# Kernel tuning notes

Hardware: AMD Instinct MI355X
Metric: run time of the kernel (lower is better)

Reference implementation:

```python
import jax, jax.numpy as jnp
import numpy as np

NHEAD = 12
EPS = 1e-5


def layernorm_nobias(x, gamma):
    mu = jnp.mean(x, axis=-1, keepdims=True)
    var = jnp.var(x, axis=-1, keepdims=True)
    return (x - mu) * jax.lax.rsqrt(var + EPS) * gamma


def setup_inputs() -> dict:
    key = jax.random.key(0)
    ks = jax.random.split(key, 10)
    b, l, d = 4, 2048, 768
    s = d ** -0.5
    return {
        "x": jax.random.normal(ks[0], (b, l, d), jnp.float32),
        "Wq": jax.random.normal(ks[1], (d, d), jnp.float32) * s,
        "Wk": jax.random.normal(ks[2], (d, d), jnp.float32) * s,
        "bk": jax.random.normal(ks[3], (d,), jnp.float32) * 0.02,
        "Wv": jax.random.normal(ks[4], (d, d), jnp.float32) * s,
        "bv": jax.random.normal(ks[5], (d,), jnp.float32) * 0.02,
        "gq": jnp.ones((d,), jnp.float32),
        "gk": jnp.ones((d,), jnp.float32),
        "Wo": jax.random.normal(ks[6], (d, d), jnp.float32) * s,
        "bo": jnp.zeros((d,), jnp.float32),
    }


def reference(x, Wq, Wk, bk, Wv, bv, gq, gk, Wo, bo):
    b, l, d = x.shape
    n = NHEAD
    hd = d // n
    scale = hd ** -0.5
    # projections (torch Linear: x @ W.T + b), QK-norm over full dmodel
    q = layernorm_nobias(x @ Wq.T, gq)
    k = layernorm_nobias(x @ Wk.T + bk, gk)
    v = x @ Wv.T + bv
    # split heads: b l (n hd) -> b n l hd
    q = q.reshape(b, l, n, hd).transpose(0, 2, 1, 3)
    k = k.reshape(b, l, n, hd).transpose(0, 2, 1, 3)
    v = v.reshape(b, l, n, hd).transpose(0, 2, 1, 3)
    # scores [b, n, l_q, l_k]; NOTE: softmax over the QUERY axis (dim=-2)
    scores = jnp.einsum('bnqd,bnkd->bnqk', q, k) * scale
    attn = jax.nn.softmax(scores, axis=-2)
    o = jnp.einsum('bnqk,bnkd->bnqd', attn, v)
    o = o.transpose(0, 2, 1, 3).reshape(b, l, d)
    return o @ Wo.T + bo + x
```

## Files before the change

kernel.cpp:

```cpp
#include <hip/hip_runtime.h>
#include <cstddef>
#include <cstdint>


typedef unsigned short u16;
typedef short  bf16x8 __attribute__((ext_vector_type(8)));
typedef float  f32x4  __attribute__((ext_vector_type(4)));
typedef unsigned short u16x8 __attribute__((ext_vector_type(8)));
typedef unsigned short u16x4 __attribute__((ext_vector_type(4)));

#define B_   4
#define L_   2048
#define D_   768
#define NH_  12
#define HD_  64
#define M_   (B_*L_)
#define SC2  (0.125f * 1.44269504088896f)

__device__ __forceinline__ float ex2(float x) { return __builtin_amdgcn_exp2f(x); }

__device__ __forceinline__ u16 f2bf(float f) {
    union { float f; unsigned u; } v; v.f = f;
    unsigned r = v.u + 0x7FFFu + ((v.u >> 16) & 1u);
    return (u16)(r >> 16);
}
__device__ __forceinline__ float bf2f(u16 b) {
    union { unsigned u; float f; } v; v.u = ((unsigned)b) << 16;
    return v.f;
}
__device__ __forceinline__ unsigned fbits(float f) {
    union { float f; unsigned u; } v; v.f = f; return v.u;
}
__device__ __forceinline__ unsigned packbf(float lo, float hi) {
    return __builtin_amdgcn_perm(fbits(hi), fbits(lo), 0x07060302u);
}

__device__ __forceinline__ void gld16(const void* g, void* l) {
    __builtin_amdgcn_global_load_lds(
        (const __attribute__((address_space(1))) unsigned*)g,
        (__attribute__((address_space(3))) unsigned*)l, 16, 0, 0);
}

__global__ __launch_bounds__(256) void cvt_bf16_kernel(
    const float* __restrict__ X, u16* __restrict__ Y, int n8)
{
    int i = blockIdx.x * 256 + threadIdx.x;
    if (i >= n8) return;
    const float4* xp = (const float4*)X + (size_t)i * 2;
    float4 a = xp[0], b = xp[1];
    u16x8 o;
    o[0] = f2bf(a.x); o[1] = f2bf(a.y); o[2] = f2bf(a.z); o[3] = f2bf(a.w);
    o[4] = f2bf(b.x); o[5] = f2bf(b.y); o[6] = f2bf(b.z); o[7] = f2bf(b.w);
    *((u16x8*)Y + i) = o;
}

__global__ __launch_bounds__(256) void cvt4_bf16_kernel(
    const float* __restrict__ W0, const float* __restrict__ W1,
    const float* __restrict__ W2, const float* __restrict__ W3,
    u16* __restrict__ Y0, u16* __restrict__ Y1,
    u16* __restrict__ Y2, u16* __restrict__ Y3, int n8)
{
    const float* X; u16* Y;
    switch (blockIdx.y) {
        case 0: X = W0; Y = Y0; break;
        case 1: X = W1; Y = Y1; break;
        case 2: X = W2; Y = Y2; break;
        default: X = W3; Y = Y3; break;
    }
    int i = blockIdx.x * 256 + threadIdx.x;
    if (i >= n8) return;
    const float4* xp = (const float4*)X + (size_t)i * 2;
    float4 a = xp[0], b = xp[1];
    u16x8 o;
    o[0] = f2bf(a.x); o[1] = f2bf(a.y); o[2] = f2bf(a.z); o[3] = f2bf(a.w);
    o[4] = f2bf(b.x); o[5] = f2bf(b.y); o[6] = f2bf(b.z); o[7] = f2bf(b.w);
    *((u16x8*)Y + i) = o;
}

__global__ __launch_bounds__(256) void gemm_qkv(
    const u16* __restrict__ A,
    const u16* __restrict__ W0, const u16* __restrict__ W1,
    const u16* __restrict__ W2,
    const float* __restrict__ bk, const float* __restrict__ bv,
    float* __restrict__ q32, float* __restrict__ k32, u16* __restrict__ vb)
{
    __shared__ __align__(16) u16 As[128 * 32];
    __shared__ __align__(16) u16 Bs[128 * 32];
    const int tid  = threadIdx.x;
    const int lane = tid & 63, w = tid >> 6;
    const int s    = lane & 15, quad = lane >> 4;
    const int seg  = blockIdx.x / 6;
    const int bn   = (blockIdx.x % 6) * 128;
    const int bm   = blockIdx.y * 128;
    const u16* W = (seg == 0) ? W0 : ((seg == 1) ? W1 : W2);
    const int mh = (w >> 1) * 64, nh = (w & 1) * 64;
    const int wb = tid & ~63;
    f32x4 acc[4][4];
    #pragma unroll
    for (int i = 0; i < 4; ++i)
        #pragma unroll
        for (int j = 0; j < 4; ++j) acc[i][j] = (f32x4){0.f, 0.f, 0.f, 0.f};

    for (int k0 = 0; k0 < D_; k0 += 32) {
        {
            int c = tid, r = c >> 2, cc = c & 3;
            gld16(A + (size_t)(bm + r) * D_ + k0 + cc * 8, As + (size_t)wb * 8);
            gld16(W + (size_t)(bn + r) * D_ + k0 + cc * 8, Bs + (size_t)wb * 8);
            c = tid + 256; r = c >> 2; cc = c & 3;
            gld16(A + (size_t)(bm + r) * D_ + k0 + cc * 8, As + (size_t)(wb + 256) * 8);
            gld16(W + (size_t)(bn + r) * D_ + k0 + cc * 8, Bs + (size_t)(wb + 256) * 8);
        }
        __syncthreads();
        bf16x8 af[4], bf[4];
        #pragma unroll
        for (int i = 0; i < 4; ++i)
            af[i] = *(const bf16x8*)(As + (mh + i * 16 + s) * 32 + quad * 8);
        #pragma unroll
        for (int j = 0; j < 4; ++j)
            bf[j] = *(const bf16x8*)(Bs + (nh + j * 16 + s) * 32 + quad * 8);
        #pragma unroll
        for (int i = 0; i < 4; ++i)
            #pragma unroll
            for (int j = 0; j < 4; ++j)
                acc[i][j] = __builtin_amdgcn_mfma_f32_16x16x32_bf16(
                    af[i], bf[j], acc[i][j], 0, 0, 0);
        __syncthreads();
    }
    #pragma unroll
    for (int j = 0; j < 4; ++j) {
        const int n = bn + nh + j * 16 + s;
        float bb = 0.0f;
        if (seg == 1) bb = bk[n];
        else if (seg == 2) bb = bv[n];
        #pragma unroll
        for (int i = 0; i < 4; ++i) {
            const int m0 = bm + mh + i * 16 + quad * 4;
            #pragma unroll
            for (int r = 0; r < 4; ++r) {
                float y = acc[i][j][r] + bb;
                const size_t idx = (size_t)(m0 + r) * D_ + n;
                if (seg == 0)      q32[idx] = y;
                else if (seg == 1) k32[idx] = y;
                else               vb[idx]  = f2bf(y);
            }
        }
    }
}

__global__ __launch_bounds__(256) void gemm_final(
    const u16* __restrict__ A, const u16* __restrict__ W,
    const float* __restrict__ bias, const float* __restrict__ resid,
    float* __restrict__ outf)
{
    __shared__ __align__(16) u16 As[128 * 32];
    __shared__ __align__(16) u16 Bs[128 * 32];
    const int tid  = threadIdx.x;
    const int lane = tid & 63, w = tid >> 6;
    const int s    = lane & 15, quad = lane >> 4;
    const int bm   = blockIdx.y * 128, bn = blockIdx.x * 128;
    const int mh   = (w >> 1) * 64, nh = (w & 1) * 64;
    const int wb   = tid & ~63;
    f32x4 acc[4][4];
    #pragma unroll
    for (int i = 0; i < 4; ++i)
        #pragma unroll
        for (int j = 0; j < 4; ++j) acc[i][j] = (f32x4){0.f, 0.f, 0.f, 0.f};

    for (int k0 = 0; k0 < D_; k0 += 32) {
        {
            int c = tid, r = c >> 2, cc = c & 3;
            gld16(A + (size_t)(bm + r) * D_ + k0 + cc * 8, As + (size_t)wb * 8);
            gld16(W + (size_t)(bn + r) * D_ + k0 + cc * 8, Bs + (size_t)wb * 8);
            c = tid + 256; r = c >> 2; cc = c & 3;
            gld16(A + (size_t)(bm + r) * D_ + k0 + cc * 8, As + (size_t)(wb + 256) * 8);
            gld16(W + (size_t)(bn + r) * D_ + k0 + cc * 8, Bs + (size_t)(wb + 256) * 8);
        }
        __syncthreads();
        bf16x8 af[4], bf[4];
        #pragma unroll
        for (int i = 0; i < 4; ++i)
            af[i] = *(const bf16x8*)(As + (mh + i * 16 + s) * 32 + quad * 8);
        #pragma unroll
        for (int j = 0; j < 4; ++j)
            bf[j] = *(const bf16x8*)(Bs + (nh + j * 16 + s) * 32 + quad * 8);
        #pragma unroll
        for (int i = 0; i < 4; ++i)
            #pragma unroll
            for (int j = 0; j < 4; ++j)
                acc[i][j] = __builtin_amdgcn_mfma_f32_16x16x32_bf16(
                    af[i], bf[j], acc[i][j], 0, 0, 0);
        __syncthreads();
    }
    #pragma unroll
    for (int j = 0; j < 4; ++j) {
        const int n = bn + nh + j * 16 + s;
        const float bb = bias[n];
        #pragma unroll
        for (int i = 0; i < 4; ++i) {
            const int m0 = bm + mh + i * 16 + quad * 4;
            #pragma unroll
            for (int r = 0; r < 4; ++r) {
                const size_t idx = (size_t)(m0 + r) * D_ + n;
                outf[idx] = acc[i][j][r] + bb + resid[idx];
            }
        }
    }
}

__global__ __launch_bounds__(256) void ln_bf16(
    const float* __restrict__ X, const float* __restrict__ gamma,
    u16* __restrict__ Y, float scale)
{
    const int row = blockIdx.x;
    const float* x = X + (size_t)row * D_;
    const int tid = threadIdx.x;
    float v[3];
    float lsum = 0.f, lsq = 0.f;
    #pragma unroll
    for (int e = 0; e < 3; ++e) {
        float t = x[tid + e * 256];
        v[e] = t; lsum += t; lsq += t * t;
    }
    #pragma unroll
    for (int off = 32; off > 0; off >>= 1) {
        lsum += __shfl_down(lsum, off);
        lsq  += __shfl_down(lsq,  off);
    }
    __shared__ float s1[4], s2[4];
    const int wv = tid >> 6, lane = tid & 63;
    if (lane == 0) { s1[wv] = lsum; s2[wv] = lsq; }
    __syncthreads();
    const float sum = s1[0] + s1[1] + s1[2] + s1[3];
    const float sq  = s2[0] + s2[1] + s2[2] + s2[3];
    const float mu  = sum * (1.0f / D_);
    const float var = sq * (1.0f / D_) - mu * mu;
    const float inv = rsqrtf(var + 1e-5f) * scale;
    #pragma unroll
    for (int e = 0; e < 3; ++e) {
        int c = tid + e * 256;
        Y[(size_t)row * D_ + c] = f2bf((v[e] - mu) * inv * gamma[c]);
    }
}

__global__ __launch_bounds__(256) void attn_stats(
    const u16* __restrict__ Qb, const u16* __restrict__ Kb,
    float* __restrict__ Rl)
{
    __shared__ __align__(16) u16 Ks[128 * 64];
    __shared__ __align__(16) u16 Qs[2][128 * 64];
    __shared__ float lbuf[4][64];
    const int tid  = threadIdx.x;
    const int lane = tid & 63, w = tid >> 6;
    const int s    = lane & 15, quad = lane >> 4;
    const int s7   = s & 7;
    const int bh   = blockIdx.y;
    const int b    = bh / NH_, h = bh % NH_;
    const int kbase = blockIdx.x * 128;
    const u16* Qg = Qb + (size_t)b * L_ * D_ + h * HD_;
    const u16* Kg = Kb + (size_t)b * L_ * D_ + h * HD_;
    const int mh = (w >> 1) * 64;
    const int nh = (w & 1) * 64;
    const int wb = tid & ~63;

    #pragma unroll
    for (int c0 = 0; c0 < 1024; c0 += 256) {
        int c = c0 + tid, r = c >> 3, cc = (c & 7) ^ (r & 7);
        gld16(Kg + (size_t)(kbase + r) * D_ + cc * 8, Ks + (size_t)(c0 + wb) * 8);
        gld16(Qg + (size_t)r * D_ + cc * 8, Qs[0] + (size_t)(c0 + wb) * 8);
    }
    __syncthreads();
    bf16x8 kf[2][4];
    #pragma unroll
    for (int kk = 0; kk < 2; ++kk)
        #pragma unroll
        for (int i = 0; i < 4; ++i)
            kf[kk][i] = *(const bf16x8*)(Ks + (mh + i * 16 + s) * 64 +
                                         ((kk * 4 + quad) ^ s7) * 8);
    float lacc[4][4];
    #pragma unroll
    for (int i = 0; i < 4; ++i)
        #pragma unroll
        for (int r = 0; r < 4; ++r) lacc[i][r] = 0.f;

    for (int t = 0; t < 16; ++t) {
        if (t < 15) {
            const int qn = (t + 1) * 128;
            u16* Qd = Qs[(t + 1) & 1];
            #pragma unroll
            for (int c0 = 0; c0 < 1024; c0 += 256) {
                int c = c0 + tid, r = c >> 3, cc = (c & 7) ^ (r & 7);
                gld16(Qg + (size_t)(qn + r) * D_ + cc * 8, Qd + (size_t)(c0 + wb) * 8);
            }
        }
        const u16* Qt = Qs[t & 1];
        f32x4 acc[4][4];
        #pragma unroll
        for (int i = 0; i < 4; ++i)
            #pragma unroll
            for (int j = 0; j < 4; ++j) acc[i][j] = (f32x4){0.f, 0.f, 0.f, 0.f};
        #pragma unroll
        for (int kk = 0; kk < 2; ++kk) {
            bf16x8 bf[4];
            #pragma unroll
            for (int j = 0; j < 4; ++j)
                bf[j] = *(const bf16x8*)(Qt + (nh + j * 16 + s) * 64 +
                                         ((kk * 4 + quad) ^ s7) * 8);
            #pragma unroll
            for (int i = 0; i < 4; ++i)
                #pragma unroll
                for (int j = 0; j < 4; ++j)
                    acc[i][j] = __builtin_amdgcn_mfma_f32_16x16x32_bf16(
                        kf[kk][i], bf[j], acc[i][j], 0, 0, 0);
        }
        #pragma unroll
        for (int i = 0; i < 4; ++i)
            #pragma unroll
            for (int r = 0; r < 4; ++r) {
                float l0 = ex2(acc[i][0][r]) + ex2(acc[i][1][r]);
                float l1 = ex2(acc[i][2][r]) + ex2(acc[i][3][r]);
                lacc[i][r] += l0 + l1;
            }
        __syncthreads();
    }
    #pragma unroll
    for (int i = 0; i < 4; ++i)
        #pragma unroll
        for (int r = 0; r < 4; ++r) {
            float v = lacc[i][r];
            #pragma unroll
            for (int d2 = 1; d2 < 16; d2 <<= 1) v += __shfl_xor(v, d2);
            lacc[i][r] = v;
        }
    if (s == 0) {
        #pragma unroll
        for (int i = 0; i < 4; ++i)
            #pragma unroll
            for (int r = 0; r < 4; ++r)
                lbuf[w][i * 16 + quad * 4 + r] = lacc[i][r];
    }
    __syncthreads();
    if (tid < 128) {
        int kh = tid >> 6, kl = tid & 63;
        float l = lbuf[kh * 2][kl] + lbuf[kh * 2 + 1][kl];
        Rl[(size_t)bh * L_ + kbase + tid] = 1.0f / l;
    }
}

__global__ __launch_bounds__(256) void transpose_v_scaled(
    const u16* __restrict__ Vb, const float* __restrict__ Rl,
    u16* __restrict__ Vt)
{
    const int l0 = blockIdx.x * 64, h = blockIdx.y, b = blockIdx.z;
    const int bh = b * NH_ + h;
    __shared__ __align__(16) u16 Ts[64][72];
    const int tid = threadIdx.x;
    #pragma unroll
    for (int c = tid; c < 512; c += 256) {
        int r = c >> 3, cc = c & 7;
        u16x8 val = *(const u16x8*)(Vb + (size_t)(b * L_ + l0 + r) * D_ + h * HD_ + cc * 8);
        const float rl = Rl[(size_t)bh * L_ + l0 + r];
        #pragma unroll
        for (int e = 0; e < 8; ++e) val[e] = f2bf(bf2f(val[e]) * rl);
        *(u16x8*)(&Ts[r][cc * 8]) = val;
    }
    __syncthreads();
    const int d = tid >> 2, lc = (tid & 3) * 16;
    u16 tmp[16];
    #pragma unroll
    for (int e = 0; e < 16; ++e) tmp[e] = Ts[lc + e][d];
    u16* dst = Vt + ((size_t)bh * HD_ + d) * L_ + l0 + (lc & 32) + ((lc >> 4) & 1) * 4;
    #pragma unroll
    for (int qd = 0; qd < 4; ++qd) {
        u16x4 o;
        #pragma unroll
        for (int e = 0; e < 4; ++e) o[e] = tmp[qd * 4 + e];
        *(u16x4*)(dst + qd * 8) = o;
    }
}

__global__ __launch_bounds__(256, 2) void attn_out(
    const u16* __restrict__ Qb, const u16* __restrict__ Kb,
    const u16* __restrict__ Vt, u16* __restrict__ Ob)
{
    __shared__ __align__(16) u16 Qs[256 * 64];
    __shared__ __align__(16) u16 Ks[2][64 * 64];
    __shared__ __align__(16) u16 Vts[2][64 * 64];
    const int tid  = threadIdx.x;
    const int lane = tid & 63, w = tid >> 6;
    const int s    = lane & 15, quad = lane >> 4;
    const int s7   = s & 7;
    const int bh   = blockIdx.y;
    const int b    = bh / NH_, h = bh % NH_;
    const int qbase = blockIdx.x * 256;
    const int qw   = w * 64;
    const u16* Qg = Qb + (size_t)b * L_ * D_ + h * HD_;
    const u16* Kg = Kb + (size_t)b * L_ * D_ + h * HD_;
    const u16* Vg = Vt + (size_t)bh * HD_ * L_;
    const int wb = tid & ~63;

    #pragma unroll
    for (int c0 = 0; c0 < 2048; c0 += 256) {
        int c = c0 + tid, r = c >> 3, cc = (c & 7) ^ (r & 7);
        gld16(Qg + (size_t)(qbase + r) * D_ + cc * 8, Qs + (size_t)(c0 + wb) * 8);
    }
    {
        int c = tid, r = c >> 3, cc = (c & 7) ^ (r & 7);
        gld16(Kg + (size_t)r * D_ + cc * 8, Ks[0] + (size_t)wb * 8);
        gld16(Vg + (size_t)r * L_ + cc * 8, Vts[0] + (size_t)wb * 8);
        c = tid + 256; r = c >> 3; cc = (c & 7) ^ (r & 7);
        gld16(Kg + (size_t)r * D_ + cc * 8, Ks[0] + (size_t)(wb + 256) * 8);
        gld16(Vg + (size_t)r * L_ + cc * 8, Vts[0] + (size_t)(wb + 256) * 8);
    }
    __syncthreads();
    bf16x8 qf[2][4];
    #pragma unroll
    for (int kk = 0; kk < 2; ++kk)
        #pragma unroll
        for (int j = 0; j < 4; ++j)
            qf[kk][j] = *(const bf16x8*)(Qs + (qw + j * 16 + s) * 64 +
                                         ((kk * 4 + quad) ^ s7) * 8);
    f32x4 acc_o[4][4];
    #pragma unroll
    for (int i = 0; i < 4; ++i)
        #pragma unroll
        for (int j = 0; j < 4; ++j) acc_o[i][j] = (f32x4){0.f, 0.f, 0.f, 0.f};

    for (int t = 0; t < 32; ++t) {
        const u16* Kt  = Ks[t & 1];
        const u16* Vtt = Vts[t & 1];
        if (t < 31) {
            const int kn = (t + 1) * 64;
            u16* Kd = Ks[(t + 1) & 1];
            u16* Vd = Vts[(t + 1) & 1];
            int c = tid, r = c >> 3, cc = (c & 7) ^ (r & 7);
            gld16(Kg + (size_t)(kn + r) * D_ + cc * 8, Kd + (size_t)wb * 8);
            gld16(Vg + (size_t)r * L_ + kn + cc * 8,   Vd + (size_t)wb * 8);
            c = tid + 256; r = c >> 3; cc = (c & 7) ^ (r & 7);
            gld16(Kg + (size_t)(kn + r) * D_ + cc * 8, Kd + (size_t)(wb + 256) * 8);
            gld16(Vg + (size_t)r * L_ + kn + cc * 8,   Vd + (size_t)(wb + 256) * 8);
        }
        f32x4 acc_s[4][4];
        #pragma unroll
        for (int i = 0; i < 4; ++i)
            #pragma unroll
            for (int j = 0; j < 4; ++j) acc_s[i][j] = (f32x4){0.f, 0.f, 0.f, 0.f};
        #pragma unroll
        for (int kk = 0; kk < 2; ++kk) {
            bf16x8 kfr[4];
            #pragma unroll
            for (int i = 0; i < 4; ++i)
                kfr[i] = *(const bf16x8*)(Kt + (i * 16 + s) * 64 +
                                          ((kk * 4 + quad) ^ s7) * 8);
            #pragma unroll
            for (int i = 0; i < 4; ++i)
                #pragma unroll
                for (int j = 0; j < 4; ++j)
                    acc_s[i][j] = __builtin_amdgcn_mfma_f32_16x16x32_bf16(
                        kfr[i], qf[kk][j], acc_s[i][j], 0, 0, 0);
        }
        unsigned pk[4][4][2];
        #pragma unroll
        for (int i = 0; i < 4; ++i)
            #pragma unroll
            for (int j = 0; j < 4; ++j) {
                float p0 = ex2(acc_s[i][j][0]), p1 = ex2(acc_s[i][j][1]);
                float p2 = ex2(acc_s[i][j][2]), p3 = ex2(acc_s[i][j][3]);
                pk[i][j][0] = packbf(p0, p1);
                pk[i][j][1] = packbf(p2, p3);
            }
        #pragma unroll
        for (int kk = 0; kk < 2; ++kk) {
            bf16x8 av[4];
            #pragma unroll
            for (int i = 0; i < 4; ++i)
                av[i] = *(const bf16x8*)(Vtt + (i * 16 + s) * 64 +
                                         ((kk * 4 + quad) ^ s7) * 8);
            #pragma unroll
            for (int j = 0; j < 4; ++j) {
                union { unsigned u[4]; bf16x8 v; } bu;
                bu.u[0] = pk[2 * kk][j][0];
                bu.u[1] = pk[2 * kk][j][1];
                bu.u[2] = pk[2 * kk + 1][j][0];
                bu.u[3] = pk[2 * kk + 1][j][1];
                #pragma unroll
                for (int i = 0; i < 4; ++i)
                    acc_o[i][j] = __builtin_amdgcn_mfma_f32_16x16x32_bf16(
                        av[i], bu.v, acc_o[i][j], 0, 0, 0);
            }
        }
        __syncthreads();
    }
    #pragma unroll
    for (int i = 0; i < 4; ++i) {
        const int d0 = i * 16 + quad * 4;
        const int dchunk = i * 2 + (quad >> 1), doff = (quad & 1) * 4;
        #pragma unroll
        for (int j = 0; j < 4; ++j) {
            const int q = qw + j * 16 + s;
            u16x4 ov;
            #pragma unroll
            for (int r = 0; r < 4; ++r) ov[r] = f2bf(acc_o[i][j][r]);
            *(u16x4*)(Qs + q * 64 + (dchunk ^ s7) * 8 + doff) = ov;
        }
    }
    __syncthreads();
    {
        const int q7 = tid & 7;
        u16* dst = Ob + (size_t)(b * L_ + qbase + tid) * D_ + h * HD_;
        #pragma unroll
        for (int c = 0; c < 8; ++c) {
            u16x8 v = *(const u16x8*)(Qs + tid * 64 + ((c ^ q7) * 8));
            *(u16x8*)(dst + c * 8) = v;
        }
    }
}

extern "C" void kernel_launch(void* const* d_in, const int* in_sizes, int n_in,
                              void* d_out, int out_size, void* d_ws, size_t ws_size,
                              hipStream_t stream)
{
    const float* x  = (const float*)d_in[0];
    const float* Wq = (const float*)d_in[1];
    const float* Wk = (const float*)d_in[2];
    const float* bk = (const float*)d_in[3];
    const float* Wv = (const float*)d_in[4];
    const float* bv = (const float*)d_in[5];
    const float* gq = (const float*)d_in[6];
    const float* gk = (const float*)d_in[7];
    const float* Wo = (const float*)d_in[8];
    const float* bo = (const float*)d_in[9];
    float* out = (float*)d_out;

    char* p = (char*)d_ws;
    float* q32 = (float*)p;  p += (size_t)M_ * D_ * 4;
    float* k32 = (float*)p;  p += (size_t)M_ * D_ * 4;
    u16* xb  = (u16*)p;      p += (size_t)M_ * D_ * 2;
    u16* qb  = (u16*)p;      p += (size_t)M_ * D_ * 2;
    u16* kb  = (u16*)p;      p += (size_t)M_ * D_ * 2;
    u16* vb  = (u16*)p;      p += (size_t)M_ * D_ * 2;
    u16* wqb = (u16*)p;      p += (size_t)D_ * D_ * 2;
    u16* wkb = (u16*)p;      p += (size_t)D_ * D_ * 2;
    u16* wvb = (u16*)p;      p += (size_t)D_ * D_ * 2;
    u16* wob = (u16*)p;      p += (size_t)D_ * D_ * 2;
    float* Rl = (float*)p;   p += (size_t)B_ * NH_ * L_ * 4;
    u16* ob = (u16*)q32;
    u16* vt = (u16*)k32;

    const int nX = M_ * D_, nW = D_ * D_;
    cvt_bf16_kernel<<<nX / 2048, 256, 0, stream>>>(x, xb, nX / 8);
    cvt4_bf16_kernel<<<dim3(nW / 2048, 4), 256, 0, stream>>>(
        Wq, Wk, Wv, Wo, wqb, wkb, wvb, wob, nW / 8);

    gemm_qkv<<<dim3(18, M_ / 128), 256, 0, stream>>>(
        xb, wqb, wkb, wvb, bk, bv, q32, k32, vb);

    ln_bf16<<<M_, 256, 0, stream>>>(q32, gq, qb, SC2);
    ln_bf16<<<M_, 256, 0, stream>>>(k32, gk, kb, 1.0f);

    dim3 sgrid(L_ / 128, B_ * NH_);
    attn_stats<<<sgrid, 256, 0, stream>>>(qb, kb, Rl);
    transpose_v_scaled<<<dim3(L_ / 64, NH_, B_), 256, 0, stream>>>(vb, Rl, vt);
    dim3 ogrid(L_ / 256, B_ * NH_);
    attn_out<<<ogrid, 256, 0, stream>>>(qb, kb, vt, ob);

    gemm_final<<<dim3(D_ / 128, M_ / 128), 256, 0, stream>>>(ob, wob, bo, x, out);
}
```

Measured before the change: 314.8 us.

## Double-buffer GEMM tiles, swizzle LDS, and store pre-norm Q/K in bf16

```diff
diff --git a/kernel.cpp b/kernel.cpp
--- a/kernel.cpp
+++ b/kernel.cpp
@@ -82,10 +82,10 @@
     const u16* __restrict__ W0, const u16* __restrict__ W1,
     const u16* __restrict__ W2,
     const float* __restrict__ bk, const float* __restrict__ bv,
-    float* __restrict__ q32, float* __restrict__ k32, u16* __restrict__ vb)
-{
-    __shared__ __align__(16) u16 As[128 * 32];
-    __shared__ __align__(16) u16 Bs[128 * 32];
+    u16* __restrict__ q_o, u16* __restrict__ k_o, u16* __restrict__ v_o)
+{
+    __shared__ __align__(16) u16 lds[16384];
+    __shared__ float bs[128];
     const int tid  = threadIdx.x;
     const int lane = tid & 63, w = tid >> 6;
     const int s    = lane & 15, quad = lane >> 4;
@@ -93,56 +93,83 @@
     const int bn   = (blockIdx.x % 6) * 128;
     const int bm   = blockIdx.y * 128;
     const u16* W = (seg == 0) ? W0 : ((seg == 1) ? W1 : W2);
+    u16* OUT = (seg == 0) ? q_o : ((seg == 1) ? k_o : v_o);
     const int mh = (w >> 1) * 64, nh = (w & 1) * 64;
     const int wb = tid & ~63;
+    const int cq = quad ^ ((s >> 1) & 3);
+
+    if (tid < 128)
+        bs[tid] = (seg == 1) ? bk[bn + tid] : ((seg == 2) ? bv[bn + tid] : 0.0f);
+
     f32x4 acc[4][4];
     #pragma unroll
-    for (int i = 0; i < 4; ++i)
-        #pragma unroll
-        for (int j = 0; j < 4; ++j) acc[i][j] = (f32x4){0.f, 0.f, 0.f, 0.f};
-
-    for (int k0 = 0; k0 < D_; k0 += 32) {
-        {
-            int c = tid, r = c >> 2, cc = c & 3;
-            gld16(A + (size_t)(bm + r) * D_ + k0 + cc * 8, As + (size_t)wb * 8);
-            gld16(W + (size_t)(bn + r) * D_ + k0 + cc * 8, Bs + (size_t)wb * 8);
-            c = tid + 256; r = c >> 2; cc = c & 3;
-            gld16(A + (size_t)(bm + r) * D_ + k0 + cc * 8, As + (size_t)(wb + 256) * 8);
-            gld16(W + (size_t)(bn + r) * D_ + k0 + cc * 8, Bs + (size_t)(wb + 256) * 8);
-        }
+    for (int j = 0; j < 4; ++j)
+        #pragma unroll
+        for (int i = 0; i < 4; ++i) acc[j][i] = (f32x4){0.f, 0.f, 0.f, 0.f};
+
+    {
+        int c = tid, r = c >> 2, cs = (c & 3) ^ ((r >> 1) & 3);
+        gld16(A + (size_t)(bm + r) * D_ + cs * 8, lds + (size_t)wb * 8);
+        gld16(W + (size_t)(bn + r) * D_ + cs * 8, lds + 8192 + (size_t)wb * 8);
+        c = tid + 256; r = c >> 2; cs = (c & 3) ^ ((r >> 1) & 3);
+        gld16(A + (size_t)(bm + r) * D_ + cs * 8, lds + (size_t)(wb + 256) * 8);
+        gld16(W + (size_t)(bn + r) * D_ + cs * 8, lds + 8192 + (size_t)(wb + 256) * 8);
+    }
+    __syncthreads();
+
+    for (int t = 0; t < 24; ++t) {
+        const u16* Ab = lds + (t & 1) * 4096;
+        const u16* Bb = lds + 8192 + (t & 1) * 4096;
+        if (t < 23) {
+            const int k0 = (t + 1) * 32;
+            u16* Ad = lds + ((t + 1) & 1) * 4096;
+            u16* Bd = lds + 8192 + ((t + 1) & 1) * 4096;
+            int c = tid, r = c >> 2, cs = (c & 3) ^ ((r >> 1) & 3);
+            gld16(A + (size_t)(bm + r) * D_ + k0 + cs * 8, Ad + (size_t)wb * 8);
+            gld16(W + (size_t)(bn + r) * D_ + k0 + cs * 8, Bd + (size_t)wb * 8);
+            c = tid + 256; r = c >> 2; cs = (c & 3) ^ ((r >> 1) & 3);
+            gld16(A + (size_t)(bm + r) * D_ + k0 + cs * 8, Ad + (size_t)(wb + 256) * 8);
+            gld16(W + (size_t)(bn + r) * D_ + k0 + cs * 8, Bd + (size_t)(wb + 256) * 8);
+        }
+        bf16x8 af[4], bf[4];
+        #pragma unroll
+        for (int i = 0; i < 4; ++i)
+            af[i] = *(const bf16x8*)(Ab + (mh + i * 16 + s) * 32 + cq * 8);
+        #pragma unroll
+        for (int j = 0; j < 4; ++j)
+            bf[j] = *(const bf16x8*)(Bb + (nh + j * 16 + s) * 32 + cq * 8);
+        #pragma unroll
+        for (int j = 0; j < 4; ++j)
+            #pragma unroll
+            for (int i = 0; i < 4; ++i)
+                acc[j][i] = __builtin_amdgcn_mfma_f32_16x16x32_bf16(
+                    bf[j], af[i], acc[j][i], 0, 0, 0);
         __syncthreads();
-        bf16x8 af[4], bf[4];
-        #pragma unroll
-        for (int i = 0; i < 4; ++i)
-            af[i] = *(const bf16x8*)(As + (mh + i * 16 + s) * 32 + quad * 8);
-        #pragma unroll
-        for (int j = 0; j < 4; ++j)
-            bf[j] = *(const bf16x8*)(Bs + (nh + j * 16 + s) * 32 + quad * 8);
-        #pragma unroll
-        for (int i = 0; i < 4; ++i)
-            #pragma unroll
-            for (int j = 0; j < 4; ++j)
-                acc[i][j] = __builtin_amdgcn_mfma_f32_16x16x32_bf16(
-                    af[i], bf[j], acc[i][j], 0, 0, 0);
-        __syncthreads();
-    }
+    }
+    u16* Ct = lds;
     #pragma unroll
     for (int j = 0; j < 4; ++j) {
-        const int n = bn + nh + j * 16 + s;
-        float bb = 0.0f;
-        if (seg == 1) bb = bk[n];
-        else if (seg == 2) bb = bv[n];
+        const int n0 = nh + j * 16 + quad * 4;
+        const f32x4 b4 = *(const f32x4*)(bs + n0);
+        const int cn = n0 >> 3, off = n0 & 7;
         #pragma unroll
         for (int i = 0; i < 4; ++i) {
-            const int m0 = bm + mh + i * 16 + quad * 4;
-            #pragma unroll
-            for (int r = 0; r < 4; ++r) {
-                float y = acc[i][j][r] + bb;
-                const size_t idx = (size_t)(m0 + r) * D_ + n;
-                if (seg == 0)      q32[idx] = y;
-                else if (seg == 1) k32[idx] = y;
-                else               vb[idx]  = f2bf(y);
-            }
+            const int m = mh + i * 16 + s;
+            u16x4 ov;
+            #pragma unroll
+            for (int r = 0; r < 4; ++r) ov[r] = f2bf(acc[j][i][r] + b4[r]);
+            *(u16x4*)(Ct + m * 128 + ((cn ^ (m & 15)) * 8) + off) = ov;
+        }
+    }
+    __syncthreads();
+    {
+        const int m = tid >> 1, half = tid & 1;
+        u16* dst = OUT + (size_t)(bm + m) * D_ + bn + half * 64;
+        #pragma unroll
+        for (int cc = 0; cc < 8; ++cc) {
+            const int cn = half * 8 + cc;
+            u16x8 v = *(const u16x8*)(Ct + m * 128 + ((cn ^ (m & 15)) * 8));
+            *(u16x8*)(dst + cc * 8) = v;
         }
     }
 }
@@ -152,73 +179,90 @@
     const float* __restrict__ bias, const float* __restrict__ resid,
     float* __restrict__ outf)
 {
-    __shared__ __align__(16) u16 As[128 * 32];
-    __shared__ __align__(16) u16 Bs[128 * 32];
+    __shared__ __align__(16) u16 lds[16384];
     const int tid  = threadIdx.x;
     const int lane = tid & 63, w = tid >> 6;
     const int s    = lane & 15, quad = lane >> 4;
     const int bm   = blockIdx.y * 128, bn = blockIdx.x * 128;
     const int mh   = (w >> 1) * 64, nh = (w & 1) * 64;
     const int wb   = tid & ~63;
+    const int cq   = quad ^ ((s >> 1) & 3);
     f32x4 acc[4][4];
     #pragma unroll
-    for (int i = 0; i < 4; ++i)
-        #pragma unroll
-        for (int j = 0; j < 4; ++j) acc[i][j] = (f32x4){0.f, 0.f, 0.f, 0.f};
-
-    for (int k0 = 0; k0 < D_; k0 += 32) {
-        {
-            int c = tid, r = c >> 2, cc = c & 3;
-            gld16(A + (size_t)(bm + r) * D_ + k0 + cc * 8, As + (size_t)wb * 8);
-            gld16(W + (size_t)(bn + r) * D_ + k0 + cc * 8, Bs + (size_t)wb * 8);
-            c = tid + 256; r = c >> 2; cc = c & 3;
-            gld16(A + (size_t)(bm + r) * D_ + k0 + cc * 8, As + (size_t)(wb + 256) * 8);
-            gld16(W + (size_t)(bn + r) * D_ + k0 + cc * 8, Bs + (size_t)(wb + 256) * 8);
-        }
+    for (int j = 0; j < 4; ++j)
+        #pragma unroll
+        for (int i = 0; i < 4; ++i) acc[j][i] = (f32x4){0.f, 0.f, 0.f, 0.f};
+
+    {
+        int c = tid, r = c >> 2, cs = (c & 3) ^ ((r >> 1) & 3);
+        gld16(A + (size_t)(bm + r) * D_ + cs * 8, lds + (size_t)wb * 8);
+        gld16(W + (size_t)(bn + r) * D_ + cs * 8, lds + 8192 + (size_t)wb * 8);
+        c = tid + 256; r = c >> 2; cs = (c & 3) ^ ((r >> 1) & 3);
+        gld16(A + (size_t)(bm + r) * D_ + cs * 8, lds + (size_t)(wb + 256) * 8);
+        gld16(W + (size_t)(bn + r) * D_ + cs * 8, lds + 8192 + (size_t)(wb + 256) * 8);
+    }
+    __syncthreads();
+
+    for (int t = 0; t < 24; ++t) {
+        const u16* Ab = lds + (t & 1) * 4096;
+        const u16* Bb = lds + 8192 + (t & 1) * 4096;
+        if (t < 23) {
+            const int k0 = (t + 1) * 32;
+            u16* Ad = lds + ((t + 1) & 1) * 4096;
+            u16* Bd = lds + 8192 + ((t + 1) & 1) * 4096;
+            int c = tid, r = c >> 2, cs = (c & 3) ^ ((r >> 1) & 3);
+            gld16(A + (size_t)(bm + r) * D_ + k0 + cs * 8, Ad + (size_t)wb * 8);
+            gld16(W + (size_t)(bn + r) * D_ + k0 + cs * 8, Bd + (size_t)wb * 8);
+            c = tid + 256; r = c >> 2; cs = (c & 3) ^ ((r >> 1) & 3);
+            gld16(A + (size_t)(bm + r) * D_ + k0 + cs * 8, Ad + (size_t)(wb + 256) * 8);
+            gld16(W + (size_t)(bn + r) * D_ + k0 + cs * 8, Bd + (size_t)(wb + 256) * 8);
+        }
+        bf16x8 af[4], bf[4];
+        #pragma unroll
+        for (int i = 0; i < 4; ++i)
+            af[i] = *(const bf16x8*)(Ab + (mh + i * 16 + s) * 32 + cq * 8);
+        #pragma unroll
+        for (int j = 0; j < 4; ++j)
+            bf[j] = *(const bf16x8*)(Bb + (nh + j * 16 + s) * 32 + cq * 8);
+        #pragma unroll
+        for (int j = 0; j < 4; ++j)
+            #pragma unroll
+            for (int i = 0; i < 4; ++i)
+                acc[j][i] = __builtin_amdgcn_mfma_f32_16x16x32_bf16(
+                    bf[j], af[i], acc[j][i], 0, 0, 0);
         __syncthreads();
-        bf16x8 af[4], bf[4];
-        #pragma unroll
-        for (int i = 0; i < 4; ++i)
-            af[i] = *(const bf16x8*)(As + (mh + i * 16 + s) * 32 + quad * 8);
-        #pragma unroll
-        for (int j = 0; j < 4; ++j)
-            bf[j] = *(const bf16x8*)(Bs + (nh + j * 16 + s) * 32 + quad * 8);
-        #pragma unroll
-        for (int i = 0; i < 4; ++i)
-            #pragma unroll
-            for (int j = 0; j < 4; ++j)
-                acc[i][j] = __builtin_amdgcn_mfma_f32_16x16x32_bf16(
-                    af[i], bf[j], acc[i][j], 0, 0, 0);
-        __syncthreads();
     }
     #pragma unroll
     for (int j = 0; j < 4; ++j) {
-        const int n = bn + nh + j * 16 + s;
-        const float bb = bias[n];
+        const int n0 = nh + j * 16 + quad * 4;
+        const float4 b4 = *(const float4*)(bias + bn + n0);
         #pragma unroll
         for (int i = 0; i < 4; ++i) {
-            const int m0 = bm + mh + i * 16 + quad * 4;
-            #pragma unroll
-            for (int r = 0; r < 4; ++r) {
-                const size_t idx = (size_t)(m0 + r) * D_ + n;
-                outf[idx] = acc[i][j][r] + bb + resid[idx];
-            }
+            const int m = mh + i * 16 + s;
+            const size_t base = (size_t)(bm + m) * D_ + bn + n0;
+            const float4 rs = *(const float4*)(resid + base);
+            float4 o;
+            o.x = acc[j][i][0] + b4.x + rs.x;
+            o.y = acc[j][i][1] + b4.y + rs.y;
+            o.z = acc[j][i][2] + b4.z + rs.z;
+            o.w = acc[j][i][3] + b4.w + rs.w;
+            *(float4*)(outf + base) = o;
         }
     }
 }
 
 __global__ __launch_bounds__(256) void ln_bf16(
-    const float* __restrict__ X, const float* __restrict__ gamma,
+    const u16* __restrict__ X, const float* __restrict__ gamma,
     u16* __restrict__ Y, float scale)
 {
     const int row = blockIdx.x;
-    const float* x = X + (size_t)row * D_;
+    const u16* x = X + (size_t)row * D_;
     const int tid = threadIdx.x;
     float v[3];
     float lsum = 0.f, lsq = 0.f;
     #pragma unroll
     for (int e = 0; e < 3; ++e) {
-        float t = x[tid + e * 256];
+        float t = bf2f(x[tid + e * 256]);
         v[e] = t; lsum += t; lsq += t * t;
     }
     #pragma unroll
@@ -492,7 +536,6 @@
     }
     #pragma unroll
     for (int i = 0; i < 4; ++i) {
-        const int d0 = i * 16 + quad * 4;
         const int dchunk = i * 2 + (quad >> 1), doff = (quad & 1) * 4;
         #pragma unroll
         for (int j = 0; j < 4; ++j) {
@@ -532,19 +575,19 @@
     float* out = (float*)d_out;
 
     char* p = (char*)d_ws;
-    float* q32 = (float*)p;  p += (size_t)M_ * D_ * 4;
-    float* k32 = (float*)p;  p += (size_t)M_ * D_ * 4;
-    u16* xb  = (u16*)p;      p += (size_t)M_ * D_ * 2;
-    u16* qb  = (u16*)p;      p += (size_t)M_ * D_ * 2;
-    u16* kb  = (u16*)p;      p += (size_t)M_ * D_ * 2;
-    u16* vb  = (u16*)p;      p += (size_t)M_ * D_ * 2;
-    u16* wqb = (u16*)p;      p += (size_t)D_ * D_ * 2;
-    u16* wkb = (u16*)p;      p += (size_t)D_ * D_ * 2;
-    u16* wvb = (u16*)p;      p += (size_t)D_ * D_ * 2;
-    u16* wob = (u16*)p;      p += (size_t)D_ * D_ * 2;
-    float* Rl = (float*)p;   p += (size_t)B_ * NH_ * L_ * 4;
-    u16* ob = (u16*)q32;
-    u16* vt = (u16*)k32;
+    u16* xb   = (u16*)p;  p += (size_t)M_ * D_ * 2;
+    u16* qpre = (u16*)p;  p += (size_t)M_ * D_ * 2;
+    u16* kpre = (u16*)p;  p += (size_t)M_ * D_ * 2;
+    u16* vb   = (u16*)p;  p += (size_t)M_ * D_ * 2;
+    u16* qb   = (u16*)p;  p += (size_t)M_ * D_ * 2;
+    u16* kb   = (u16*)p;  p += (size_t)M_ * D_ * 2;
+    u16* wqb  = (u16*)p;  p += (size_t)D_ * D_ * 2;
+    u16* wkb  = (u16*)p;  p += (size_t)D_ * D_ * 2;
+    u16* wvb  = (u16*)p;  p += (size_t)D_ * D_ * 2;
+    u16* wob  = (u16*)p;  p += (size_t)D_ * D_ * 2;
+    float* Rl = (float*)p; p += (size_t)B_ * NH_ * L_ * 4;
+    u16* ob = qpre;
+    u16* vt = kpre;
 
     const int nX = M_ * D_, nW = D_ * D_;
     cvt_bf16_kernel<<<nX / 2048, 256, 0, stream>>>(x, xb, nX / 8);
@@ -552,10 +595,10 @@
         Wq, Wk, Wv, Wo, wqb, wkb, wvb, wob, nW / 8);
 
     gemm_qkv<<<dim3(18, M_ / 128), 256, 0, stream>>>(
-        xb, wqb, wkb, wvb, bk, bv, q32, k32, vb);
-
-    ln_bf16<<<M_, 256, 0, stream>>>(q32, gq, qb, SC2);
-    ln_bf16<<<M_, 256, 0, stream>>>(k32, gk, kb, 1.0f);
+        xb, wqb, wkb, wvb, bk, bv, qpre, kpre, vb);
+
+    ln_bf16<<<M_, 256, 0, stream>>>(qpre, gq, qb, SC2);
+    ln_bf16<<<M_, 256, 0, stream>>>(kpre, gk, kb, 1.0f);
 
     dim3 sgrid(L_ / 128, B_ * NH_);
     attn_stats<<<sgrid, 256, 0, stream>>>(qb, kb, Rl);
```

Result: slower. 325.8 us (+3.5%).
